# Kernel optimization log

Hardware: AMD Instinct MI355X
Metric: run time of the kernel (lower is better)

Reference implementation:

```python
import jax, jax.numpy as jnp
import numpy as np

NUM_HEADS = 16

def setup_inputs() -> dict:
    key = jax.random.key(0)
    k1, k2, k3 = jax.random.split(key, 3)
    B, S, H = 2, 2048, 1024
    hidden_states = jax.random.normal(k1, (B, S, H), dtype=jnp.float32)
    # nn.Linear default init scale ~ 1/sqrt(fan_in); keep magnitudes sane
    w_qkv = jax.random.normal(k2, (3 * H, H), dtype=jnp.float32) * (1.0 / np.sqrt(H))
    w_o = jax.random.normal(k3, (H, H), dtype=jnp.float32) * (1.0 / np.sqrt(H))
    return {"hidden_states": hidden_states, "w_qkv": w_qkv, "w_o": w_o}

def reference(hidden_states, w_qkv, w_o):
    B, S, H = hidden_states.shape
    nh = NUM_HEADS
    hd = H // nh
    scale = 1.0 / np.sqrt(hd)
    # fused QKV projection: [B,S,3H]
    qkv = jnp.einsum('bsh,oh->bso', hidden_states, w_qkv)
    qkv = qkv.reshape(B, S, 3, nh, hd)
    q = qkv[:, :, 0].transpose(0, 2, 1, 3)  # [B, nh, S, hd]
    k = qkv[:, :, 1].transpose(0, 2, 1, 3)
    v = qkv[:, :, 2].transpose(0, 2, 1, 3)
    # scaled dot-product attention (math identical to the online-softmax path)
    scores = jnp.einsum('bhqd,bhkd->bhqk', q, k) * scale
    probs = jax.nn.softmax(scores, axis=-1)
    attn = jnp.einsum('bhqk,bhkd->bhqd', probs, v)  # [B, nh, S, hd]
    attn = attn.transpose(0, 2, 1, 3).reshape(B, S, H)
    out = jnp.einsum('bsh,oh->bso', attn, w_o)
    return out
```

## Files before the change

kernel.cpp:

```cpp
#include <hip/hip_runtime.h>

using f32x4 = __attribute__((ext_vector_type(4))) float;
using s16x8 = __attribute__((ext_vector_type(8))) short;
using u16x8 = __attribute__((ext_vector_type(8))) unsigned short;
using u16x4 = __attribute__((ext_vector_type(4))) unsigned short;
using u32x2 = __attribute__((ext_vector_type(2))) unsigned int;

__device__ __forceinline__ unsigned short f2bf(float f) {
  union { float f; unsigned u; } v; v.f = f;
  return (unsigned short)((v.u + 0x7FFFu + ((v.u >> 16) & 1u)) >> 16);
}

__device__ __forceinline__ unsigned pk2bf(float a, float b) {
#if __has_builtin(__builtin_amdgcn_cvt_pk_bf16_f32)
  typedef __bf16 bf2 __attribute__((ext_vector_type(2)));
  union { bf2 v; unsigned u; } c;
  c.v = __builtin_amdgcn_cvt_pk_bf16_f32(a, b);
  return c.u;
#else
  return (unsigned)f2bf(a) | ((unsigned)f2bf(b) << 16);
#endif
}

__device__ __forceinline__ f32x4 fzero4() {
  f32x4 z; z[0] = 0.f; z[1] = 0.f; z[2] = 0.f; z[3] = 0.f; return z;
}

__device__ __forceinline__ void gl_lds16(const void* g, void* l) {
  __builtin_amdgcn_global_load_lds(
      (const __attribute__((address_space(1))) unsigned int*)g,
      (__attribute__((address_space(3))) unsigned int*)l, 16, 0, 0);
}

__global__ __launch_bounds__(256) void cvt_bf16(const float* __restrict__ h,
                                                const float* __restrict__ wq,
                                                const float* __restrict__ wo,
                                                unsigned short* __restrict__ dst) {
  const int blk = blockIdx.x;
  const float* src;
  if (blk < 2048) src = h;
  else if (blk < 3584) src = wq - 4194304;
  else src = wo - (4194304 + 3145728);
  const size_t i = (size_t)blk * 2048 + threadIdx.x * 8;
  f32x4 a0 = *(const f32x4*)(src + i);
  f32x4 a1 = *(const f32x4*)(src + i + 4);
  u32x2 v0, v1;
  v0[0] = pk2bf(a0[0], a0[1]); v0[1] = pk2bf(a0[2], a0[3]);
  v1[0] = pk2bf(a1[0], a1[1]); v1[1] = pk2bf(a1[2], a1[3]);
  *(u32x2*)(dst + i) = v0;
  *(u32x2*)(dst + i + 4) = v1;
}

template <int CMODE>
__global__ __launch_bounds__(256) void gemm_bt(const unsigned short* __restrict__ A,
                                               const unsigned short* __restrict__ B,
                                               void* __restrict__ Cp,
                                               void* __restrict__ Vgp,
                                               int M, int N, int K) {
  __shared__ unsigned short As[128 * 64];
  __shared__ unsigned short Bs[128 * 64];
  const int t = threadIdx.x;
  const int lane = t & 63, wid = t >> 6;
  const int l15 = lane & 15, quad = lane >> 4;
  const int bm = blockIdx.x * 128, bn = blockIdx.y * 128;
  const int wm = (wid >> 1) * 64, wn = (wid & 1) * 64;
  const int wbase = t & ~63;

  f32x4 acc[4][4];
#pragma unroll
  for (int i = 0; i < 4; ++i)
#pragma unroll
    for (int j = 0; j < 4; ++j) acc[i][j] = fzero4();

  for (int k0 = 0; k0 < K; k0 += 64) {
    __syncthreads();
#pragma unroll
    for (int i = 0; i < 4; ++i) {
      const int dc = t + i * 256;
      const int row = dc >> 3, cp = dc & 7;
      const int cl = cp ^ (row & 7);
      gl_lds16(A + (size_t)(bm + row) * K + k0 + cl * 8, &As[(size_t)(i * 256 + wbase) * 8]);
      gl_lds16(B + (size_t)(bn + row) * K + k0 + cl * 8, &Bs[(size_t)(i * 256 + wbase) * 8]);
    }
    __syncthreads();
#pragma unroll
    for (int c = 0; c < 2; ++c) {
      s16x8 af[4], bf[4];
#pragma unroll
      for (int mt = 0; mt < 4; ++mt) {
        const int row = wm + mt * 16 + l15;
        af[mt] = *(const s16x8*)&As[row * 64 + (((c * 4 + quad) ^ (l15 & 7)) * 8)];
      }
#pragma unroll
      for (int nt = 0; nt < 4; ++nt) {
        const int row = wn + nt * 16 + l15;
        bf[nt] = *(const s16x8*)&Bs[row * 64 + (((c * 4 + quad) ^ (l15 & 7)) * 8)];
      }
#pragma unroll
      for (int mt = 0; mt < 4; ++mt)
#pragma unroll
        for (int nt = 0; nt < 4; ++nt)
          acc[mt][nt] = __builtin_amdgcn_mfma_f32_16x16x32_bf16(af[mt], bf[nt], acc[mt][nt], 0, 0, 0);
    }
  }

  if (CMODE == 2 && bn >= 2048) {
#pragma unroll
    for (int mt = 0; mt < 4; ++mt)
#pragma unroll
      for (int nt = 0; nt < 4; ++nt) {
        const int row0 = bm + wm + mt * 16 + quad * 4;
        const int c = bn + wn + nt * 16 + l15 - 2048;
        const int b = row0 >> 11, s = row0 & 2047;
        u32x2 ov;
        ov[0] = pk2bf(acc[mt][nt][0], acc[mt][nt][1]);
        ov[1] = pk2bf(acc[mt][nt][2], acc[mt][nt][3]);
        *(u32x2*)&((unsigned short*)Vgp)[(size_t)b * (1024 * 2048) + (size_t)c * 2048 + s] = ov;
      }
    return;
  }

  const float qscale = (CMODE == 2 && bn < 1024) ? 0.18033688011112042f : 1.0f;
#pragma unroll
  for (int mt = 0; mt < 4; ++mt)
#pragma unroll
    for (int nt = 0; nt < 4; ++nt)
#pragma unroll
      for (int r = 0; r < 4; ++r) {
        const int row = bm + wm + mt * 16 + quad * 4 + r;
        const int col = bn + wn + nt * 16 + l15;
        if (CMODE == 0)
          ((float*)Cp)[(size_t)row * N + col] = acc[mt][nt][r];
        else
          ((unsigned short*)Cp)[(size_t)row * 2048 + col] = f2bf(acc[mt][nt][r] * qscale);
      }
}

__global__ __launch_bounds__(256) void gemm_bt_n64(const unsigned short* __restrict__ A,
                                                   const unsigned short* __restrict__ B,
                                                   float* __restrict__ C,
                                                   int M, int N, int K) {
  __shared__ unsigned short As[128 * 64];
  __shared__ unsigned short Bs[64 * 64];
  const int t = threadIdx.x;
  const int lane = t & 63, wid = t >> 6;
  const int l15 = lane & 15, quad = lane >> 4;
  const int bm = blockIdx.x * 128, bn = blockIdx.y * 64;
  const int wm = (wid >> 1) * 64, wn = (wid & 1) * 32;
  const int wbase = t & ~63;

  f32x4 acc[4][2];
#pragma unroll
  for (int i = 0; i < 4; ++i)
#pragma unroll
    for (int j = 0; j < 2; ++j) acc[i][j] = fzero4();

  for (int k0 = 0; k0 < K; k0 += 64) {
    __syncthreads();
#pragma unroll
    for (int i = 0; i < 4; ++i) {
      const int dc = t + i * 256;
      const int row = dc >> 3, cp = dc & 7;
      const int cl = cp ^ (row & 7);
      gl_lds16(A + (size_t)(bm + row) * K + k0 + cl * 8, &As[(size_t)(i * 256 + wbase) * 8]);
    }
#pragma unroll
    for (int i = 0; i < 2; ++i) {
      const int dc = t + i * 256;
      const int row = dc >> 3, cp = dc & 7;
      const int cl = cp ^ (row & 7);
      gl_lds16(B + (size_t)(bn + row) * K + k0 + cl * 8, &Bs[(size_t)(i * 256 + wbase) * 8]);
    }
    __syncthreads();
#pragma unroll
    for (int c = 0; c < 2; ++c) {
      s16x8 af[4], bf[2];
#pragma unroll
      for (int mt = 0; mt < 4; ++mt) {
        const int row = wm + mt * 16 + l15;
        af[mt] = *(const s16x8*)&As[row * 64 + (((c * 4 + quad) ^ (l15 & 7)) * 8)];
      }
#pragma unroll
      for (int nt = 0; nt < 2; ++nt) {
        const int row = wn + nt * 16 + l15;
        bf[nt] = *(const s16x8*)&Bs[row * 64 + (((c * 4 + quad) ^ (l15 & 7)) * 8)];
      }
#pragma unroll
      for (int mt = 0; mt < 4; ++mt)
#pragma unroll
        for (int nt = 0; nt < 2; ++nt)
          acc[mt][nt] = __builtin_amdgcn_mfma_f32_16x16x32_bf16(af[mt], bf[nt], acc[mt][nt], 0, 0, 0);
    }
  }

#pragma unroll
  for (int mt = 0; mt < 4; ++mt)
#pragma unroll
    for (int nt = 0; nt < 2; ++nt)
#pragma unroll
      for (int r = 0; r < 4; ++r) {
        const int row = bm + wm + mt * 16 + quad * 4 + r;
        const int col = bn + wn + nt * 16 + l15;
        C[(size_t)row * N + col] = acc[mt][nt][r];
      }
}

__global__ __launch_bounds__(256) void fattn(const unsigned short* __restrict__ qk,
                                             const unsigned short* __restrict__ vg,
                                             unsigned short* __restrict__ attn) {
  constexpr int S = 2048, H = 1024, LD = 2048, HD = 64;
  __shared__ unsigned short Ks[2][64 * 64];
  __shared__ unsigned short Vt[2][64 * 64];
  __shared__ unsigned short Pn[4][32][72];

  const int t = threadIdx.x, lane = t & 63, wid = t >> 6;
  const int l15 = lane & 15, quad = lane >> 4;
  const int h = blockIdx.x >> 1, b = blockIdx.x & 1, qt = blockIdx.y;
  const unsigned short* qbase = qk + (size_t)b * S * LD;
  const unsigned short* kbase = qbase + 1024 + h * HD;
  const unsigned short* vbase = vg + ((size_t)b * 16 + h) * HD * S;
  const int qrow0 = qt * 128;
  const int wbase = t & ~63;

  s16x8 qf[2][2];
#pragma unroll
  for (int nt = 0; nt < 2; ++nt)
#pragma unroll
    for (int c = 0; c < 2; ++c)
      qf[nt][c] = *(const s16x8*)(qbase + (size_t)(qrow0 + wid * 32 + nt * 16 + l15) * LD +
                                  h * HD + c * 32 + quad * 8);

  s16x8 ones;
#pragma unroll
  for (int j = 0; j < 8; ++j) ones[j] = (short)0x3F80;

  f32x4 o[4][2], lacc[2];
#pragma unroll
  for (int i = 0; i < 4; ++i)
#pragma unroll
    for (int j = 0; j < 2; ++j) o[i][j] = fzero4();
  lacc[0] = fzero4(); lacc[1] = fzero4();

  auto stage = [&](int kt, int bu) {
#pragma unroll
    for (int i = 0; i < 2; ++i) {
      const int pos = t + i * 256;
      const int row = pos >> 3, s = pos & 7;
      const int clog = s ^ (row & 7);
      gl_lds16(kbase + (size_t)(kt * 64 + row) * LD + clog * 8,
               &Ks[bu][(size_t)(i * 256 + wbase) * 8]);
      gl_lds16(vbase + (size_t)row * S + kt * 64 + clog * 8,
               &Vt[bu][(size_t)(i * 256 + wbase) * 8]);
    }
  };

  stage(0, 0);
  __syncthreads();

  for (int kt = 0; kt < S / 64; ++kt) {
    const int cur = kt & 1;
    if (kt < S / 64 - 1) stage(kt + 1, cur ^ 1);

    const unsigned short* K = Ks[cur];
    const unsigned short* V = Vt[cur];

    f32x4 st[4][2];
#pragma unroll
    for (int i = 0; i < 4; ++i)
#pragma unroll
      for (int j = 0; j < 2; ++j) st[i][j] = fzero4();
#pragma unroll
    for (int c = 0; c < 2; ++c) {
      s16x8 kf[4];
#pragma unroll
      for (int mt = 0; mt < 4; ++mt)
        kf[mt] = *(const s16x8*)&K[(mt * 16 + l15) * 64 + ((c * 4 + quad) ^ (l15 & 7)) * 8];
#pragma unroll
      for (int mt = 0; mt < 4; ++mt)
#pragma unroll
        for (int nt = 0; nt < 2; ++nt)
          st[mt][nt] = __builtin_amdgcn_mfma_f32_16x16x32_bf16(kf[mt], qf[nt][c], st[mt][nt], 0, 0, 0);
    }

#pragma unroll
    for (int mt = 0; mt < 4; ++mt)
#pragma unroll
      for (int nt = 0; nt < 2; ++nt)
#pragma unroll
        for (int r = 0; r < 4; ++r) st[mt][nt][r] = __builtin_amdgcn_exp2f(st[mt][nt][r]);

#pragma unroll
    for (int mt = 0; mt < 4; ++mt)
#pragma unroll
      for (int nt = 0; nt < 2; ++nt) {
        u32x2 pk;
        pk[0] = pk2bf(st[mt][nt][0], st[mt][nt][1]);
        pk[1] = pk2bf(st[mt][nt][2], st[mt][nt][3]);
        *(u32x2*)&Pn[wid][nt * 16 + l15][mt * 16 + quad * 4] = pk;
      }

#pragma unroll
    for (int c = 0; c < 2; ++c) {
      s16x8 pf[2];
#pragma unroll
      for (int nt = 0; nt < 2; ++nt) {
        pf[nt] = *(const s16x8*)&Pn[wid][nt * 16 + l15][c * 32 + quad * 8];
        lacc[nt] = __builtin_amdgcn_mfma_f32_16x16x32_bf16(ones, pf[nt], lacc[nt], 0, 0, 0);
      }
#pragma unroll
      for (int mt = 0; mt < 4; ++mt) {
        s16x8 vf = *(const s16x8*)&V[(mt * 16 + l15) * 64 + ((c * 4 + quad) ^ (l15 & 7)) * 8];
#pragma unroll
        for (int nt = 0; nt < 2; ++nt)
          o[mt][nt] = __builtin_amdgcn_mfma_f32_16x16x32_bf16(vf, pf[nt], o[mt][nt], 0, 0, 0);
      }
    }

    __syncthreads();
  }

#pragma unroll
  for (int nt = 0; nt < 2; ++nt) {
    const float inv = 1.f / lacc[nt][0];
    const int row = b * S + qrow0 + wid * 32 + nt * 16 + l15;
#pragma unroll
    for (int mt = 0; mt < 4; ++mt) {
      u32x2 ov;
      ov[0] = pk2bf(o[mt][nt][0] * inv, o[mt][nt][1] * inv);
      ov[1] = pk2bf(o[mt][nt][2] * inv, o[mt][nt][3] * inv);
      *(u32x2*)&attn[(size_t)row * H + h * HD + mt * 16 + quad * 4] = ov;
    }
  }
}

extern "C" void kernel_launch(void* const* d_in, const int* in_sizes, int n_in,
                              void* d_out, int out_size, void* d_ws, size_t ws_size,
                              hipStream_t stream) {
  const float* hidden = (const float*)d_in[0];
  const float* w_qkv = (const float*)d_in[1];
  const float* w_o = (const float*)d_in[2];
  float* out = (float*)d_out;

  constexpr int B = 2, S = 2048, H = 1024;
  constexpr int M = B * S;

  unsigned short* hbf = (unsigned short*)d_ws;
  unsigned short* wqbf = hbf + 4194304;
  unsigned short* wobf = wqbf + 3145728;
  unsigned short* qkbuf = wobf + 1048576;
  unsigned short* vg = qkbuf + (size_t)M * 2048;
  unsigned short* attn = hbf;

  dim3 blk(256);
  cvt_bf16<<<4096, blk, 0, stream>>>(hidden, w_qkv, w_o, hbf);
  gemm_bt<2><<<dim3(M / 128, (3 * H) / 128), blk, 0, stream>>>(
      hbf, wqbf, (void*)qkbuf, (void*)vg, M, 3 * H, H);
  fattn<<<dim3(32, S / 128, 1), blk, 0, stream>>>(qkbuf, vg, attn);
  gemm_bt_n64<<<dim3(M / 128, H / 64), blk, 0, stream>>>(
      attn, wobf, out, M, H, H);
}
```

Before: 177.4 us.

## Split attention over key range into two partials and add combine kernel

The flash-attention kernel now also splits each (batch, head, query-tile) along the key dimension into two halves via a third grid dimension. This doubles the block count to give more parallelism across the GPU's compute units. Each half writes an unnormalized bf16 output and its row sums, and a new combine kernel adds the two partials and normalizes before the output projection. In exchange it adds an extra launch, about 16 MB of extra global traffic, and one more bf16 rounding of the unnormalized partials. It also depends on both halves using the same softmax max reference.

```diff
diff --git a/kernel.cpp b/kernel.cpp
--- a/kernel.cpp
+++ b/kernel.cpp
@@ -9,6 +9,10 @@
 __device__ __forceinline__ unsigned short f2bf(float f) {
   union { float f; unsigned u; } v; v.f = f;
   return (unsigned short)((v.u + 0x7FFFu + ((v.u >> 16) & 1u)) >> 16);
+}
+
+__device__ __forceinline__ float bf2f(unsigned short u) {
+  union { unsigned u; float f; } v; v.u = ((unsigned)u) << 16; return v.f;
 }
 
 __device__ __forceinline__ unsigned pk2bf(float a, float b) {
@@ -205,10 +209,12 @@
       }
 }
 
-__global__ __launch_bounds__(256) void fattn(const unsigned short* __restrict__ qk,
-                                             const unsigned short* __restrict__ vg,
-                                             unsigned short* __restrict__ attn) {
-  constexpr int S = 2048, H = 1024, LD = 2048, HD = 64;
+__global__ __launch_bounds__(256) void fattn_sk(const unsigned short* __restrict__ qk,
+                                                const unsigned short* __restrict__ vg,
+                                                unsigned short* __restrict__ o0,
+                                                unsigned short* __restrict__ o1,
+                                                float* __restrict__ lpart) {
+  constexpr int S = 2048, LD = 2048, HD = 64;
   __shared__ unsigned short Ks[2][64 * 64];
   __shared__ unsigned short Vt[2][64 * 64];
   __shared__ unsigned short Pn[4][32][72];
@@ -216,6 +222,7 @@
   const int t = threadIdx.x, lane = t & 63, wid = t >> 6;
   const int l15 = lane & 15, quad = lane >> 4;
   const int h = blockIdx.x >> 1, b = blockIdx.x & 1, qt = blockIdx.y;
+  const int ks = blockIdx.z;
   const unsigned short* qbase = qk + (size_t)b * S * LD;
   const unsigned short* kbase = qbase + 1024 + h * HD;
   const unsigned short* vbase = vg + ((size_t)b * 16 + h) * HD * S;
@@ -254,21 +261,22 @@
     }
   };
 
-  stage(0, 0);
+  const int k0t = ks * 16;
+  stage(k0t, 0);
   __syncthreads();
 
-  for (int kt = 0; kt < S / 64; ++kt) {
-    const int cur = kt & 1;
-    if (kt < S / 64 - 1) stage(kt + 1, cur ^ 1);
+  for (int i = 0; i < 16; ++i) {
+    const int cur = i & 1;
+    if (i < 15) stage(k0t + i + 1, cur ^ 1);
 
     const unsigned short* K = Ks[cur];
     const unsigned short* V = Vt[cur];
 
     f32x4 st[4][2];
 #pragma unroll
-    for (int i = 0; i < 4; ++i)
-#pragma unroll
-      for (int j = 0; j < 2; ++j) st[i][j] = fzero4();
+    for (int ii = 0; ii < 4; ++ii)
+#pragma unroll
+      for (int j = 0; j < 2; ++j) st[ii][j] = fzero4();
 #pragma unroll
     for (int c = 0; c < 2; ++c) {
       s16x8 kf[4];
@@ -319,18 +327,44 @@
     __syncthreads();
   }
 
+  unsigned short* dst = ks ? o1 : o0;
 #pragma unroll
   for (int nt = 0; nt < 2; ++nt) {
-    const float inv = 1.f / lacc[nt][0];
-    const int row = b * S + qrow0 + wid * 32 + nt * 16 + l15;
+    const int q = qrow0 + wid * 32 + nt * 16 + l15;
+    const size_t row = (size_t)b * S + q;
 #pragma unroll
     for (int mt = 0; mt < 4; ++mt) {
       u32x2 ov;
-      ov[0] = pk2bf(o[mt][nt][0] * inv, o[mt][nt][1] * inv);
-      ov[1] = pk2bf(o[mt][nt][2] * inv, o[mt][nt][3] * inv);
-      *(u32x2*)&attn[(size_t)row * H + h * HD + mt * 16 + quad * 4] = ov;
-    }
-  }
+      ov[0] = pk2bf(o[mt][nt][0], o[mt][nt][1]);
+      ov[1] = pk2bf(o[mt][nt][2], o[mt][nt][3]);
+      *(u32x2*)&dst[row * 1024 + h * HD + mt * 16 + quad * 4] = ov;
+    }
+    if (quad == 0)
+      lpart[ks * 65536 + (b * 16 + h) * S + q] = lacc[nt][0];
+  }
+}
+
+__global__ __launch_bounds__(256) void combine(unsigned short* __restrict__ o0,
+                                               const unsigned short* __restrict__ o1,
+                                               const float* __restrict__ lp) {
+  const int gid = blockIdx.x * 256 + threadIdx.x;
+  const size_t i8 = (size_t)gid * 8;
+  const int row = gid >> 7;
+  const int col = (gid & 127) * 8;
+  const int h = col >> 6, b = row >> 11, s = row & 2047;
+  const int li = (b * 16 + h) * 2048 + s;
+  const float inv = 1.f / (lp[li] + lp[li + 65536]);
+  u16x8 a = *(const u16x8*)(o0 + i8);
+  u16x8 c = *(const u16x8*)(o1 + i8);
+  u32x2 r0, r1;
+  float f0 = (bf2f(a[0]) + bf2f(c[0])) * inv, f1 = (bf2f(a[1]) + bf2f(c[1])) * inv;
+  float f2 = (bf2f(a[2]) + bf2f(c[2])) * inv, f3 = (bf2f(a[3]) + bf2f(c[3])) * inv;
+  float f4 = (bf2f(a[4]) + bf2f(c[4])) * inv, f5 = (bf2f(a[5]) + bf2f(c[5])) * inv;
+  float f6 = (bf2f(a[6]) + bf2f(c[6])) * inv, f7 = (bf2f(a[7]) + bf2f(c[7])) * inv;
+  r0[0] = pk2bf(f0, f1); r0[1] = pk2bf(f2, f3);
+  r1[0] = pk2bf(f4, f5); r1[1] = pk2bf(f6, f7);
+  *(u32x2*)(o0 + i8) = r0;
+  *(u32x2*)(o0 + i8 + 4) = r1;
 }
 
 extern "C" void kernel_launch(void* const* d_in, const int* in_sizes, int n_in,
@@ -349,13 +383,16 @@
   unsigned short* wobf = wqbf + 3145728;
   unsigned short* qkbuf = wobf + 1048576;
   unsigned short* vg = qkbuf + (size_t)M * 2048;
-  unsigned short* attn = hbf;
+  unsigned short* opart1 = vg + (size_t)B * 1024 * S;
+  float* lpart = (float*)(opart1 + 4194304);
+  unsigned short* opart0 = hbf;
 
   dim3 blk(256);
   cvt_bf16<<<4096, blk, 0, stream>>>(hidden, w_qkv, w_o, hbf);
   gemm_bt<2><<<dim3(M / 128, (3 * H) / 128), blk, 0, stream>>>(
       hbf, wqbf, (void*)qkbuf, (void*)vg, M, 3 * H, H);
-  fattn<<<dim3(32, S / 128, 1), blk, 0, stream>>>(qkbuf, vg, attn);
+  fattn_sk<<<dim3(32, S / 128, 2), blk, 0, stream>>>(qkbuf, vg, opart0, opart1, lpart);
+  combine<<<2048, blk, 0, stream>>>(opart0, opart1, lpart);
   gemm_bt_n64<<<dim3(M / 128, H / 64), blk, 0, stream>>>(
-      attn, wobf, out, M, H, H);
-}
+      opart0, wobf, out, M, H, H);
+}
```

After: 192.4 us. 8.5% more time.
